# Kernel optimization log

Measured on AMD Instinct MI355X. Metric: run time of the kernel, lower is better.

## Reference

```python
import jax, jax.numpy as jnp
import numpy as np

NUM_NODES = 12
HEADS = 4
PERIOD = 24
HID = 144  # nn.LSTM(12*12, 12*12, 2)
NEG_INF = -9e15

ADJ = np.array([
    [1,0,0,0,0,1,0,0,0,0,1,1],
    [0,1,0,0,0,0,0,1,0,0,1,0],
    [0,0,1,0,0,0,1,0,0,0,0,1],
    [0,0,0,1,0,0,1,0,0,0,0,0],
    [0,0,0,0,1,1,0,0,0,0,0,0],
    [1,0,0,0,1,1,0,0,0,0,0,0],
    [0,0,1,1,0,0,1,0,0,0,1,0],
    [0,1,0,0,0,0,0,1,0,1,0,0],
    [0,0,0,0,0,0,0,0,1,1,1,1],
    [0,0,0,0,0,0,0,1,1,1,1,0],
    [1,1,0,0,0,0,1,0,1,1,1,1],
    [1,0,1,0,0,0,0,0,1,0,1,1]], dtype=np.int32)
EI, EJ = np.nonzero(ADJ)  # static edge list (row-major order, matches torch nonzero)


def gat_layer(x, W, b, a):
    # x: [B, N, c_in]; W: [c_in, H*c]; a: [H, 2c]
    B, N, _ = x.shape
    H = a.shape[0]
    h = (x @ W + b).reshape(B, N, H, -1)  # [B,N,H,c]
    # NOTE: adj has batch dim 1 in the original, so logits come from sample 0 only
    hi = h[0, EI]  # [E,H,c]
    hj = h[0, EJ]
    logits = jnp.einsum('ehc,hc->eh', jnp.concatenate([hi, hj], axis=-1), a)
    logits = jax.nn.leaky_relu(logits, 0.2)
    mat = jnp.full((N, N, H), NEG_INF, dtype=logits.dtype).at[EI, EJ].set(logits)
    probs = jax.nn.softmax(mat, axis=1)  # softmax over j (dim=2 in torch incl. batch)
    out = jnp.einsum('ijh,bjhc->bihc', probs, h)  # broadcast attn over batch
    return out.reshape(B, N, -1)  # concat heads


def lstm2(x, params, h0, c0):
    # x: [T,B,D]; params: list of (Wih,Whh,bih,bhh); h0,c0: [L,B,HID]
    hs, cs = [], []
    y = x
    for l, (Wih, Whh, bih, bhh) in enumerate(params):
        def step(carry, xt, Wih=Wih, Whh=Whh, bih=bih, bhh=bhh):
            h, c = carry
            g = xt @ Wih.T + h @ Whh.T + (bih + bhh)
            i, f, gg, o = jnp.split(g, 4, axis=-1)  # torch gate order i,f,g,o
            c2 = jax.nn.sigmoid(f) * c + jax.nn.sigmoid(i) * jnp.tanh(gg)
            h2 = jax.nn.sigmoid(o) * jnp.tanh(c2)
            return (h2, c2), h2
        (hT, cT), y = jax.lax.scan(step, (h0[l], c0[l]), y)
        hs.append(hT)
        cs.append(cT)
    return y, jnp.stack(hs), jnp.stack(cs)


def reference(x, gW0, gb0, ga0, gW1, gb1, ga1,
              eWih0, eWhh0, ebih0, ebhh0, eWih1, eWhh1, ebih1, ebhh1,
              dWih0, dWhh0, dbih0, dbhh0, dWih1, dWhh1, dbih1, dbhh1,
              gW3, gb3, ga3, gW4, gb4, ga4, fW, fb):
    B = x.shape[0]
    h = jax.nn.elu(gat_layer(x, gW0, gb0, ga0))           # [B,12,16]
    h = jax.nn.elu(gat_layer(h, gW1, gb1, ga1))           # [B,12,12]
    seq = h.reshape(PERIOD, -1, NUM_NODES * 12)            # [24, B/24, 144]
    Bb = seq.shape[1]
    z = jnp.zeros((2, Bb, HID), dtype=seq.dtype)
    enc_params = [(eWih0, eWhh0, ebih0, ebhh0), (eWih1, eWhh1, ebih1, ebhh1)]
    dec_params = [(dWih0, dWhh0, dbih0, dbhh0), (dWih1, dWhh1, dbih1, dbhh1)]
    y, hn, _ = lstm2(seq, enc_params, z, z)
    dec_in = jnp.zeros_like(y)
    y, _, _ = lstm2(dec_in, dec_params, hn, jnp.zeros_like(hn))
    h = y.reshape(-1, NUM_NODES, 12)                       # [B,12,12]
    h = jax.nn.elu(gat_layer(h, gW3, gb3, ga3))            # [B,12,16]
    h = jax.nn.elu(gat_layer(h, gW4, gb4, ga4))            # [B,12,24]
    h = h.reshape(B, NUM_NODES * 24)
    h = jax.nn.leaky_relu(h @ fW + fb, 0.01)               # fc_layers
    xr = h.reshape(B, NUM_NODES, -1)                       # [B,12,22]
    # F.mse_loss(..., reduce='sum') -> legacy truthy reduce => mean reduction
    out = jnp.mean((x - xr) ** 2, axis=(1, 2)).reshape(-1, 1)
    return out


def setup_inputs() -> dict:
    key = jax.random.key(0)
    ks = iter(jax.random.split(key, 64))
    def p(shape, s=0.2):
        return s * jax.random.normal(next(ks), shape, dtype=jnp.float32)
    B = 98304  # multiple of period=24
    d = {
        'x': jax.random.normal(next(ks), (B, 12, 22), dtype=jnp.float32),
        'gW0': p((22, 16)), 'gb0': p((16,)), 'ga0': p((4, 8)),
        'gW1': p((16, 12)), 'gb1': p((12,)), 'ga1': p((4, 6)),
    }
    for pre in ('e', 'd'):
        for l in (0, 1):
            d[f'{pre}Wih{l}'] = p((576, 144))
            d[f'{pre}Whh{l}'] = p((576, 144))
            d[f'{pre}bih{l}'] = p((576,))
            d[f'{pre}bhh{l}'] = p((576,))
    d.update({'gW3': p((12, 16)), 'gb3': p((16,)), 'ga3': p((4, 8)),
              'gW4': p((16, 24)), 'gb4': p((24,)), 'ga4': p((4, 12)),
              'fW': p((288, 264)), 'fb': p((264,))})
    return d
```

## Files before the change

kernel.cpp:

```cpp
#include <hip/hip_runtime.h>

#define DI __device__ __forceinline__

typedef short bfrag8 __attribute__((ext_vector_type(8)));
typedef float ffrag4 __attribute__((ext_vector_type(4)));

DI ushort f2b(float f){
  union { float f; unsigned u; } v; v.f = f;
  unsigned u = v.u;
  u += 0x7FFF + ((u >> 16) & 1);
  return (ushort)(u >> 16);
}
DI float b2f(ushort h){
  union { unsigned u; float f; } v; v.u = ((unsigned)h) << 16;
  return v.f;
}
DI float sigm(float x){ return 1.0f / (1.0f + __expf(-x)); }
DI float tanh_(float x){ return 1.0f - 2.0f / (1.0f + __expf(2.0f * x)); }
DI float elu_(float x){ return x > 0.f ? x : __expf(x) - 1.f; }

__global__ void k_probs(const float* xf, const ushort* xb, int in_c,
                        const float* W1, const float* b1, const float* a1, int hc1, int c1,
                        const float* W2, const float* b2, const float* a2, int hc2, int c2,
                        float* outA, float* outB)
{
  __shared__ float xs[12 * 22];
  __shared__ float h1[12 * 16];
  __shared__ float lg[4 * 144];
  __shared__ float pr[4 * 144];
  __shared__ float h1e[12 * 16];
  __shared__ float h2[12 * 24];
  const int t = threadIdx.x;
  const unsigned adj[12] = {0xC21u,0x482u,0x844u,0x048u,0x030u,0x031u,
                            0x44Cu,0x282u,0xF00u,0x780u,0xF43u,0xD05u};
  if (t < 12 * in_c){
    if (xf) xs[t] = xf[t];
    else    xs[t] = b2f(xb[t]);
  }
  __syncthreads();
  if (t < 12 * hc1){
    int i = t / hc1, o = t % hc1;
    float v = b1[o];
    for (int k = 0; k < in_c; k++) v += xs[i * in_c + k] * W1[k * hc1 + o];
    h1[t] = v;
  }
  __syncthreads();
  {
    int h = t / 144, ij = t % 144, i = ij / 12, j = ij % 12;
    float v;
    if ((adj[i] >> j) & 1){
      v = 0.f;
      for (int c = 0; c < c1; c++)
        v += a1[h*2*c1 + c] * h1[i*hc1 + h*c1 + c] + a1[h*2*c1 + c1 + c] * h1[j*hc1 + h*c1 + c];
      v = v > 0.f ? v : 0.2f * v;
    } else v = -9e15f;
    lg[t] = v;
  }
  __syncthreads();
  if (t < 48){
    int h = t / 12, i = t % 12;
    const float* row = &lg[h*144 + i*12];
    float m = row[0];
    for (int j = 1; j < 12; j++) m = fmaxf(m, row[j]);
    float e[12], s = 0.f;
    for (int j = 0; j < 12; j++){ e[j] = __expf(row[j] - m); s += e[j]; }
    float inv = 1.f / s;
    for (int j = 0; j < 12; j++){
      float p = e[j] * inv;
      pr[h*144 + i*12 + j] = p;
      outA[h*144 + i*12 + j] = p;
    }
  }
  __syncthreads();
  if (t < 12 * hc1){
    int i = t / hc1, o = t % hc1, h = o / c1;
    float v = 0.f;
    for (int j = 0; j < 12; j++) v += pr[h*144 + i*12 + j] * h1[j*hc1 + o];
    h1e[t] = elu_(v);
  }
  __syncthreads();
  if (t < 12 * hc2){
    int i = t / hc2, o = t % hc2;
    float v = b2[o];
    for (int k = 0; k < hc1; k++) v += h1e[i*hc1 + k] * W2[k*hc2 + o];
    h2[t] = v;
  }
  __syncthreads();
  {
    int h = t / 144, ij = t % 144, i = ij / 12, j = ij % 12;
    float v;
    if ((adj[i] >> j) & 1){
      v = 0.f;
      for (int c = 0; c < c2; c++)
        v += a2[h*2*c2 + c] * h2[i*hc2 + h*c2 + c] + a2[h*2*c2 + c2 + c] * h2[j*hc2 + h*c2 + c];
      v = v > 0.f ? v : 0.2f * v;
    } else v = -9e15f;
    lg[t] = v;
  }
  __syncthreads();
  if (t < 48){
    int h = t / 12, i = t % 12;
    const float* row = &lg[h*144 + i*12];
    float m = row[0];
    for (int j = 1; j < 12; j++) m = fmaxf(m, row[j]);
    float e[12], s = 0.f;
    for (int j = 0; j < 12; j++){ e[j] = __expf(row[j] - m); s += e[j]; }
    float inv = 1.f / s;
    for (int j = 0; j < 12; j++) outB[h*144 + i*12 + j] = e[j] * inv;
  }
}

__global__ void k_prep_op(const float* __restrict__ W, const float* __restrict__ p,
                          int Cin, int Cout, int hdiv, int K, int KT, int N,
                          ushort* __restrict__ dst)
{
  int bI = blockIdx.x;
  int kt = bI % KT, nt = bI / KT;
  int l = threadIdx.x, ln = l & 15, q = l >> 4;
  int n = nt * 16 + ln;
  for (int j = 0; j < 8; j++){
    int k = kt * 32 + q * 8 + j;
    float v = 0.f;
    if (k < K && n < N){
      if (p){
        int jj = k / Cin, kk = k % Cin;
        int i = n / Cout, o = n % Cout;
        v = p[(o / hdiv) * 144 + i * 12 + jj] * W[kk * Cout + o];
      } else {
        v = W[k * Cout + n];
      }
    }
    dst[((long)bI * 64 + l) * 8 + j] = f2b(v);
  }
}

__global__ void k_prep_lstm(const float* eWih0, const float* eWhh0,
                            const float* eWih1, const float* eWhh1,
                            const float* dWhh0,
                            const float* dWih1, const float* dWhh1,
                            ushort* __restrict__ dstBase)
{
  int combo = blockIdx.y;
  const float* Wh; const float* Wx; long off; int ntau;
  if (combo == 0){ Wh = eWhh0; Wx = eWih0; off = 0;      ntau = 72; }
  else if (combo == 1){ Wh = eWhh1; Wx = eWih1; off = 184320; ntau = 72; }
  else if (combo == 2){ Wh = dWhh0; Wx = dWhh0; off = 368640; ntau = 36; }
  else { Wh = dWhh1; Wx = dWih1; off = 460800; ntau = 72; }
  int bI = blockIdx.x;
  int tau = bI / 5, kt = bI % 5;
  if (tau >= ntau) return;
  const float* W = (tau < 36) ? Wh : Wx;
  int tt = (tau < 36) ? tau : tau - 36;
  int gt = tt / 9, ct = tt % 9;
  int l = threadIdx.x, ln = l & 15, q = l >> 4;
  int n = gt * 144 + ct * 16 + ln;
  ushort* d = dstBase + off;
  for (int j = 0; j < 8; j++){
    int k = kt * 32 + q * 8 + j;
    float v = (k < 144) ? W[(long)n * 144 + k] : 0.f;
    d[((long)bI * 64 + l) * 8 + j] = f2b(v);
  }
}

__global__ __launch_bounds__(512) void k_gat01(
    const float* __restrict__ x, const ushort* __restrict__ M0f, const float* __restrict__ b0,
    const ushort* __restrict__ M1f, const float* __restrict__ b1,
    ushort* __restrict__ seq)
{
  __shared__ ushort xs[128 * 288];
  __shared__ ushort h1e[128 * 200];
  int t = threadIdx.x;
  long row0 = (long)blockIdx.x * 128;
  int w = t >> 6, l = t & 63, q = l >> 4, ln = l & 15;
  if (t < 384){
    int row = t / 3, seg = t % 3;
    *(uint4*)&xs[row * 288 + 264 + seg * 8] = make_uint4(0u, 0u, 0u, 0u);
  }
  for (int idx = t; idx < 8448; idx += 512){
    int row = idx / 66, c4 = idx % 66;
    float4 v = *(const float4*)&x[(row0 + row) * 264 + c4 * 4];
    ushort4 o; o.x = f2b(v.x); o.y = f2b(v.y); o.z = f2b(v.z); o.w = f2b(v.w);
    *(ushort4*)&xs[row * 288 + c4 * 4] = o;
  }
  int nta[2] = {w, (w < 4) ? 8 + w : -1};
  bfrag8 f0[2][9];
  #pragma unroll
  for (int ii = 0; ii < 2; ii++)
    if (nta[ii] >= 0)
      #pragma unroll
      for (int kt = 0; kt < 9; kt++)
        f0[ii][kt] = *(const bfrag8*)&M0f[((long)(nta[ii] * 9 + kt) * 64 + l) * 8];
  float bias0 = b0[ln];
  __syncthreads();
  for (int rb = 0; rb < 8; rb++){
    bfrag8 af[9];
    #pragma unroll
    for (int kt = 0; kt < 9; kt++)
      af[kt] = *(const bfrag8*)&xs[(rb * 16 + ln) * 288 + kt * 32 + q * 8];
    #pragma unroll
    for (int ii = 0; ii < 2; ii++){
      if (nta[ii] < 0) continue;
      ffrag4 acc = {bias0, bias0, bias0, bias0};
      #pragma unroll
      for (int kt = 0; kt < 9; kt++)
        acc = __builtin_amdgcn_mfma_f32_16x16x32_bf16(af[kt], f0[ii][kt], acc, 0, 0, 0);
      #pragma unroll
      for (int r = 0; r < 4; r++)
        h1e[(rb * 16 + q * 4 + r) * 200 + nta[ii] * 16 + ln] = f2b(elu_(acc[r]));
    }
  }
  int ntb[2] = {w, (w == 0) ? 8 : -1};
  bfrag8 f1[2][6];
  #pragma unroll
  for (int ii = 0; ii < 2; ii++)
    if (ntb[ii] >= 0)
      #pragma unroll
      for (int kt = 0; kt < 6; kt++)
        f1[ii][kt] = *(const bfrag8*)&M1f[((long)(ntb[ii] * 6 + kt) * 64 + l) * 8];
  __syncthreads();
  for (int rb = 0; rb < 8; rb++){
    bfrag8 af[6];
    #pragma unroll
    for (int kt = 0; kt < 6; kt++)
      af[kt] = *(const bfrag8*)&h1e[(rb * 16 + ln) * 200 + kt * 32 + q * 8];
    #pragma unroll
    for (int ii = 0; ii < 2; ii++){
      if (ntb[ii] < 0) continue;
      int n = ntb[ii] * 16 + ln;
      float bias = b1[n % 12];
      ffrag4 acc = {bias, bias, bias, bias};
      #pragma unroll
      for (int kt = 0; kt < 6; kt++)
        acc = __builtin_amdgcn_mfma_f32_16x16x32_bf16(af[kt], f1[ii][kt], acc, 0, 0, 0);
      #pragma unroll
      for (int r = 0; r < 4; r++)
        xs[(rb * 16 + q * 4 + r) * 144 + n] = f2b(elu_(acc[r]));
    }
  }
  __syncthreads();
  for (int i = t; i < 2304; i += 512)
    *(uint4*)&seq[row0 * 144 + (long)i * 8] = *(uint4*)&xs[i * 8];
}

template<bool HASX>
__global__ __launch_bounds__(512, 2) void k_scan(
    const ushort* __restrict__ Wf,
    const ushort* __restrict__ seqin,
    const float* __restrict__ bih, const float* __restrict__ bhh,
    const ushort* __restrict__ h0,
    ushort* __restrict__ Y,
    ushort* __restrict__ hT)
{
  constexpr int NT = HASX ? 9 : 5;
  __shared__ ushort hl[16 * 168];
  __shared__ float P[(HASX ? 2 : 1) * 9216];
  __shared__ float bsh[576];
  int t = threadIdx.x, rbk = blockIdx.x;
  int w = t >> 6, l = t & 63, q = l >> 4, ln = l & 15;
  if (t < 336){
    int row = t / 21, ch = t % 21;
    uint4 z = make_uint4(0u, 0u, 0u, 0u);
    if (h0 && ch < 18) z = *(const uint4*)&h0[((long)rbk * 16 + row) * 144 + ch * 8];
    *(uint4*)&hl[row * 168 + ch * 8] = z;
  }
  for (int i = t; i < 576; i += 512) bsh[i] = bih[i] + bhh[i];
  bfrag8 wf[NT][5];
  #pragma unroll
  for (int i = 0; i < NT; i++){
    int tau = w + i * 8;
    int tc = (HASX || tau < 36) ? tau : 0;
    #pragma unroll
    for (int kt = 0; kt < 5; kt++)
      wf[i][kt] = *(const bfrag8*)&Wf[((long)(tc * 5 + kt) * 64 + l) * 8];
  }
  float cst[5] = {0.f, 0.f, 0.f, 0.f, 0.f};
  __syncthreads();
  for (int ts = 0; ts < 24; ts++){
    bfrag8 ah[5];
    #pragma unroll
    for (int kt = 0; kt < 5; kt++)
      ah[kt] = *(const bfrag8*)&hl[ln * 168 + kt * 32 + q * 8];
    bfrag8 ax[5];
    if (HASX){
      const ushort* xr = &seqin[(((long)ts * 4096) + (long)rbk * 16 + ln) * 144];
      #pragma unroll
      for (int kt = 0; kt < 5; kt++)
        ax[kt] = *(const bfrag8*)&xr[kt * 32 + q * 8];
    }
    #pragma unroll
    for (int i = 0; i < NT; i++){
      int tau = w + i * 8;
      if (!HASX && tau >= 36) continue;
      ffrag4 acc = {0.f, 0.f, 0.f, 0.f};
      if (HASX && tau >= 36){
        #pragma unroll
        for (int kt = 0; kt < 5; kt++)
          acc = __builtin_amdgcn_mfma_f32_16x16x32_bf16(ax[kt], wf[i][kt], acc, 0, 0, 0);
        int tt = tau - 36;
        *(float4*)&P[9216 + ((tt / 9) * 144 + (tt % 9) * 16 + ln) * 16 + q * 4] = *(float4*)&acc;
      } else {
        #pragma unroll
        for (int kt = 0; kt < 5; kt++)
          acc = __builtin_amdgcn_mfma_f32_16x16x32_bf16(ah[kt], wf[i][kt], acc, 0, 0, 0);
        *(float4*)&P[((tau / 9) * 144 + (tau % 9) * 16 + ln) * 16 + q * 4] = *(float4*)&acc;
      }
    }
    __syncthreads();
    #pragma unroll
    for (int j = 0; j < 5; j++){
      int cell = t + j * 512;
      if (cell < 2304){
        int col = cell >> 4, row = cell & 15;
        int base = col * 16 + row;
        float iv = P[base], fv = P[2304 + base], gv = P[4608 + base], ov = P[6912 + base];
        if (HASX){
          iv += P[9216 + base]; fv += P[9216 + 2304 + base];
          gv += P[9216 + 4608 + base]; ov += P[9216 + 6912 + base];
        }
        iv += bsh[col]; fv += bsh[144 + col]; gv += bsh[288 + col]; ov += bsh[432 + col];
        float cn = sigm(fv) * cst[j] + sigm(iv) * tanh_(gv);
        cst[j] = cn;
        hl[row * 168 + col] = f2b(sigm(ov) * tanh_(cn));
      }
    }
    __syncthreads();
    if (Y && t < 288){
      int row = t / 18, ch = t % 18;
      *(uint4*)&Y[(((long)ts * 4096) + (long)rbk * 16 + row) * 144 + ch * 8] =
          *(uint4*)&hl[row * 168 + ch * 8];
    }
  }
  if (hT && t < 288){
    int row = t / 18, ch = t % 18;
    *(uint4*)&hT[((long)rbk * 16 + row) * 144 + ch * 8] = *(uint4*)&hl[row * 168 + ch * 8];
  }
}

__global__ __launch_bounds__(512) void k_tail(
    const ushort* __restrict__ Ya, const ushort* __restrict__ M3f, const float* __restrict__ b3,
    const ushort* __restrict__ M4f, const float* __restrict__ b4,
    const ushort* __restrict__ fWt, const float* __restrict__ fb,
    const float* __restrict__ x, float* __restrict__ out)
{
  __shared__ ushort h3e[128 * 200];
  __shared__ ushort bufB[128 * 288];
  __shared__ float psum[128 * 8];
  ushort* ys = bufB;
  ushort* h4e = bufB;
  int t = threadIdx.x;
  long row0 = (long)blockIdx.x * 128;
  int w = t >> 6, l = t & 63, q = l >> 4, ln = l & 15;
  if (t < 256){
    int row = t / 2, seg = t % 2;
    *(uint4*)&ys[row * 160 + 144 + seg * 8] = make_uint4(0u, 0u, 0u, 0u);
  }
  for (int idx = t; idx < 2304; idx += 512){
    int row = idx / 18, ch = idx % 18;
    *(uint4*)&ys[row * 160 + ch * 8] = *(const uint4*)&Ya[(row0 + row) * 144 + (long)ch * 8];
  }
  int nta[2] = {w, (w < 4) ? 8 + w : -1};
  bfrag8 f3[2][5];
  #pragma unroll
  for (int ii = 0; ii < 2; ii++)
    if (nta[ii] >= 0)
      #pragma unroll
      for (int kt = 0; kt < 5; kt++)
        f3[ii][kt] = *(const bfrag8*)&M3f[((long)(nta[ii] * 5 + kt) * 64 + l) * 8];
  float bias3 = b3[ln];
  __syncthreads();
  for (int rb = 0; rb < 8; rb++){
    bfrag8 af[5];
    #pragma unroll
    for (int kt = 0; kt < 5; kt++)
      af[kt] = *(const bfrag8*)&ys[(rb * 16 + ln) * 160 + kt * 32 + q * 8];
    #pragma unroll
    for (int ii = 0; ii < 2; ii++){
      if (nta[ii] < 0) continue;
      ffrag4 acc = {bias3, bias3, bias3, bias3};
      #pragma unroll
      for (int kt = 0; kt < 5; kt++)
        acc = __builtin_amdgcn_mfma_f32_16x16x32_bf16(af[kt], f3[ii][kt], acc, 0, 0, 0);
      #pragma unroll
      for (int r = 0; r < 4; r++)
        h3e[(rb * 16 + q * 4 + r) * 200 + nta[ii] * 16 + ln] = f2b(elu_(acc[r]));
    }
  }
  int ntb[3] = {2 * w, 2 * w + 1, (w < 2) ? 16 + w : -1};
  bfrag8 f4[3][6];
  #pragma unroll
  for (int ii = 0; ii < 3; ii++)
    if (ntb[ii] >= 0)
      #pragma unroll
      for (int kt = 0; kt < 6; kt++)
        f4[ii][kt] = *(const bfrag8*)&M4f[((long)(ntb[ii] * 6 + kt) * 64 + l) * 8];
  __syncthreads();
  for (int rb = 0; rb < 8; rb++){
    bfrag8 af[6];
    #pragma unroll
    for (int kt = 0; kt < 6; kt++)
      af[kt] = *(const bfrag8*)&h3e[(rb * 16 + ln) * 200 + kt * 32 + q * 8];
    #pragma unroll
    for (int ii = 0; ii < 3; ii++){
      if (ntb[ii] < 0) continue;
      int n = ntb[ii] * 16 + ln;
      float bias = b4[n % 24];
      ffrag4 acc = {bias, bias, bias, bias};
      #pragma unroll
      for (int kt = 0; kt < 6; kt++)
        acc = __builtin_amdgcn_mfma_f32_16x16x32_bf16(af[kt], f4[ii][kt], acc, 0, 0, 0);
      #pragma unroll
      for (int r = 0; r < 4; r++)
        h4e[(rb * 16 + q * 4 + r) * 288 + n] = f2b(elu_(acc[r]));
    }
  }
  int ntc[3] = {2 * w, 2 * w + 1, (w == 0) ? 16 : -1};
  bfrag8 f5[3][9];
  float bias5[3] = {0.f, 0.f, 0.f};
  #pragma unroll
  for (int ii = 0; ii < 3; ii++)
    if (ntc[ii] >= 0){
      #pragma unroll
      for (int kt = 0; kt < 9; kt++)
        f5[ii][kt] = *(const bfrag8*)&fWt[((long)(ntc[ii] * 9 + kt) * 64 + l) * 8];
      int n = ntc[ii] * 16 + ln;
      bias5[ii] = (n < 264) ? fb[n] : 0.f;
    }
  __syncthreads();
  for (int rb = 0; rb < 8; rb++){
    bfrag8 af[9];
    #pragma unroll
    for (int kt = 0; kt < 9; kt++)
      af[kt] = *(const bfrag8*)&h4e[(rb * 16 + ln) * 288 + kt * 32 + q * 8];
    float s4[4] = {0.f, 0.f, 0.f, 0.f};
    #pragma unroll
    for (int ii = 0; ii < 3; ii++){
      if (ntc[ii] < 0) continue;
      ffrag4 acc = {bias5[ii], bias5[ii], bias5[ii], bias5[ii]};
      #pragma unroll
      for (int kt = 0; kt < 9; kt++)
        acc = __builtin_amdgcn_mfma_f32_16x16x32_bf16(af[kt], f5[ii][kt], acc, 0, 0, 0);
      int n = ntc[ii] * 16 + ln;
      if (n < 264){
        #pragma unroll
        for (int r = 0; r < 4; r++){
          float v = acc[r];
          v = v > 0.f ? v : 0.01f * v;
          long row = row0 + rb * 16 + q * 4 + r;
          float d = x[row * 264 + n] - v;
          s4[r] += d * d;
        }
      }
    }
    #pragma unroll
    for (int off = 1; off < 16; off <<= 1){
      #pragma unroll
      for (int r = 0; r < 4; r++) s4[r] += __shfl_xor(s4[r], off, 16);
    }
    if (ln == 0){
      #pragma unroll
      for (int r = 0; r < 4; r++) psum[(rb * 16 + q * 4 + r) * 8 + w] = s4[r];
    }
  }
  __syncthreads();
  if (t < 128){
    float s = 0.f;
    for (int k = 0; k < 8; k++) s += psum[t * 8 + k];
    out[row0 + t] = s * (1.0f / 264.0f);
  }
}

extern "C" void kernel_launch(void* const* d_in, const int* in_sizes, int n_in,
                              void* d_out, int out_size, void* d_ws, size_t ws_size,
                              hipStream_t stream)
{
  const float* x     = (const float*)d_in[0];
  const float* gW0   = (const float*)d_in[1];
  const float* gb0   = (const float*)d_in[2];
  const float* ga0   = (const float*)d_in[3];
  const float* gW1   = (const float*)d_in[4];
  const float* gb1   = (const float*)d_in[5];
  const float* ga1   = (const float*)d_in[6];
  const float* eWih0 = (const float*)d_in[7];
  const float* eWhh0 = (const float*)d_in[8];
  const float* ebih0 = (const float*)d_in[9];
  const float* ebhh0 = (const float*)d_in[10];
  const float* eWih1 = (const float*)d_in[11];
  const float* eWhh1 = (const float*)d_in[12];
  const float* ebih1 = (const float*)d_in[13];
  const float* ebhh1 = (const float*)d_in[14];
  const float* dWhh0 = (const float*)d_in[16];
  const float* dbih0 = (const float*)d_in[17];
  const float* dbhh0 = (const float*)d_in[18];
  const float* dWih1 = (const float*)d_in[19];
  const float* dWhh1 = (const float*)d_in[20];
  const float* dbih1 = (const float*)d_in[21];
  const float* dbhh1 = (const float*)d_in[22];
  const float* gW3   = (const float*)d_in[23];
  const float* gb3   = (const float*)d_in[24];
  const float* ga3   = (const float*)d_in[25];
  const float* gW4   = (const float*)d_in[26];
  const float* gb4   = (const float*)d_in[27];
  const float* ga4   = (const float*)d_in[28];
  const float* fW    = (const float*)d_in[29];
  const float* fb    = (const float*)d_in[30];

  char* ws = (char*)d_ws;
  float*  probs0 = (float*)(ws + 0);
  float*  probs1 = (float*)(ws + 2304);
  float*  probs3 = (float*)(ws + 4608);
  float*  probs4 = (float*)(ws + 6912);
  ushort* M0f    = (ushort*)(ws + 9216);
  ushort* M1f    = (ushort*)(ws + 119808);
  ushort* M3f    = (ushort*)(ws + 175104);
  ushort* M4f    = (ushort*)(ws + 236544);
  ushort* fWt    = (ushort*)(ws + 347136);
  ushort* lstmF  = (ushort*)(ws + 503808);
  ushort* seq    = (ushort*)(ws + 1794048);
  ushort* Ya     = (ushort*)(ws + 30105600);
  ushort* Yb     = (ushort*)(ws + 58417152);
  ushort* hT0    = (ushort*)(ws + 86728704);
  ushort* hT1    = (ushort*)(ws + 87908352);
  float* out = (float*)d_out;

  k_prep_lstm<<<dim3(360, 4), 64, 0, stream>>>(eWih0, eWhh0, eWih1, eWhh1,
                                               dWhh0, dWih1, dWhh1, lstmF);
  k_prep_op<<<153, 64, 0, stream>>>(fW, nullptr, 0, 264, 1, 288, 9, 264, fWt);
  k_probs<<<1, 576, 0, stream>>>(x, nullptr, 22,
                                 gW0, gb0, ga0, 16, 4,
                                 gW1, gb1, ga1, 12, 3,
                                 probs0, probs1);
  k_prep_op<<<108, 64, 0, stream>>>(gW0, probs0, 22, 16, 4, 264, 9, 192, M0f);
  k_prep_op<<<54, 64, 0, stream>>>(gW1, probs1, 16, 12, 3, 192, 6, 144, M1f);
  k_gat01<<<768, 512, 0, stream>>>(x, M0f, gb0, M1f, gb1, seq);

  k_scan<true><<<256, 512, 0, stream>>>(lstmF + 0L,      seq, ebih0, ebhh0, nullptr, Ya, hT0);
  k_scan<true><<<256, 512, 0, stream>>>(lstmF + 184320L, Ya, ebih1, ebhh1, nullptr, nullptr, hT1);
  k_scan<false><<<256, 512, 0, stream>>>(lstmF + 368640L, nullptr, dbih0, dbhh0, hT0, Yb, nullptr);
  k_scan<true><<<256, 512, 0, stream>>>(lstmF + 460800L, Yb, dbih1, dbhh1, hT1, Ya, nullptr);

  k_probs<<<1, 576, 0, stream>>>(nullptr, Ya, 12,
                                 gW3, gb3, ga3, 16, 4,
                                 gW4, gb4, ga4, 24, 6,
                                 probs3, probs4);
  k_prep_op<<<60, 64, 0, stream>>>(gW3, probs3, 12, 16, 4, 144, 5, 192, M3f);
  k_prep_op<<<108, 64, 0, stream>>>(gW4, probs4, 16, 24, 6, 192, 6, 288, M4f);
  k_tail<<<768, 512, 0, stream>>>(Ya, M3f, gb3, M4f, gb4, fWt, fb, x, out);
}
```

Before: 669.1 us.

## Warp-specialize LSTM scan: overlap input projection with recurrent gate math

The LSTM scan kernel is split into two warp groups. Four warps hold the recurrent weights and compute the gates and cell update in registers straight from the MFMA accumulators. The other four warps precompute the input projection plus bias for the next timestep into a double-buffered shared array, prefetching sequence rows two steps ahead. This removes the full shared-memory gate round trip and the second elementwise pass, and moves the x-projection off the recurrent critical path. In exchange it uses more registers per thread and more shared memory, and Y is now written as scattered 2-byte global stores instead of vectorized rows.

```diff
diff --git a/kernel.cpp b/kernel.cpp
--- a/kernel.cpp
+++ b/kernel.cpp
@@ -251,88 +251,149 @@
     ushort* __restrict__ Y,
     ushort* __restrict__ hT)
 {
-  constexpr int NT = HASX ? 9 : 5;
-  __shared__ ushort hl[16 * 168];
-  __shared__ float P[(HASX ? 2 : 1) * 9216];
-  __shared__ float bsh[576];
+  __shared__ float Px[2][11520];
+  __shared__ float P8[1280];
+  __shared__ ushort hl[2][2688];
   int t = threadIdx.x, rbk = blockIdx.x;
   int w = t >> 6, l = t & 63, q = l >> 4, ln = l & 15;
   if (t < 336){
     int row = t / 21, ch = t % 21;
     uint4 z = make_uint4(0u, 0u, 0u, 0u);
     if (h0 && ch < 18) z = *(const uint4*)&h0[((long)rbk * 16 + row) * 144 + ch * 8];
-    *(uint4*)&hl[row * 168 + ch * 8] = z;
-  }
-  for (int i = t; i < 576; i += 512) bsh[i] = bih[i] + bhh[i];
-  bfrag8 wf[NT][5];
-  #pragma unroll
-  for (int i = 0; i < NT; i++){
-    int tau = w + i * 8;
-    int tc = (HASX || tau < 36) ? tau : 0;
+    *(uint4*)&hl[0][row * 168 + ch * 8] = z;
+    *(uint4*)&hl[1][row * 168 + ch * 8] = make_uint4(0u, 0u, 0u, 0u);
+  }
+  if (w < 4){
+    bfrag8 wh[2][4][5], w8[5];
+    #pragma unroll
+    for (int ci = 0; ci < 2; ci++)
+      #pragma unroll
+      for (int gt = 0; gt < 4; gt++)
+        #pragma unroll
+        for (int kt = 0; kt < 5; kt++)
+          wh[ci][gt][kt] = *(const bfrag8*)&Wf[((long)((gt * 9 + 2 * w + ci) * 5 + kt) * 64 + l) * 8];
     #pragma unroll
     for (int kt = 0; kt < 5; kt++)
-      wf[i][kt] = *(const bfrag8*)&Wf[((long)(tc * 5 + kt) * 64 + l) * 8];
-  }
-  float cst[5] = {0.f, 0.f, 0.f, 0.f, 0.f};
-  __syncthreads();
-  for (int ts = 0; ts < 24; ts++){
-    bfrag8 ah[5];
-    #pragma unroll
-    for (int kt = 0; kt < 5; kt++)
-      ah[kt] = *(const bfrag8*)&hl[ln * 168 + kt * 32 + q * 8];
-    bfrag8 ax[5];
+      w8[kt] = *(const bfrag8*)&Wf[((long)((w * 9 + 8) * 5 + kt) * 64 + l) * 8];
+    float cst[2][4] = {};
+    float c8 = 0.f;
+    __syncthreads();
+    for (int ts = 0; ts < 24; ts++){
+      int par = ts & 1;
+      const ushort* hlr = &hl[par][0];
+      ushort* hlw = &hl[par ^ 1][0];
+      bfrag8 ah[5];
+      #pragma unroll
+      for (int kt = 0; kt < 5; kt++)
+        ah[kt] = *(const bfrag8*)&hlr[ln * 168 + kt * 32 + q * 8];
+      #pragma unroll
+      for (int ci = 0; ci < 2; ci++){
+        int ct = 2 * w + ci;
+        ffrag4 acc[4];
+        #pragma unroll
+        for (int gt = 0; gt < 4; gt++)
+          acc[gt] = *(ffrag4*)&Px[par][(gt * 144 + ct * 16 + ln) * 20 + q * 4];
+        #pragma unroll
+        for (int gt = 0; gt < 4; gt++)
+          #pragma unroll
+          for (int kt = 0; kt < 5; kt++)
+            acc[gt] = __builtin_amdgcn_mfma_f32_16x16x32_bf16(ah[kt], wh[ci][gt][kt], acc[gt], 0, 0, 0);
+        #pragma unroll
+        for (int r = 0; r < 4; r++){
+          float cn = sigm(acc[1][r]) * cst[ci][r] + sigm(acc[0][r]) * tanh_(acc[2][r]);
+          cst[ci][r] = cn;
+          ushort hb = f2b(sigm(acc[3][r]) * tanh_(cn));
+          hlw[(q * 4 + r) * 168 + ct * 16 + ln] = hb;
+          if (Y) Y[(((long)ts * 4096) + rbk * 16 + q * 4 + r) * 144 + ct * 16 + ln] = hb;
+        }
+      }
+      {
+        ffrag4 a8 = *(ffrag4*)&Px[par][(w * 144 + 128 + ln) * 20 + q * 4];
+        #pragma unroll
+        for (int kt = 0; kt < 5; kt++)
+          a8 = __builtin_amdgcn_mfma_f32_16x16x32_bf16(ah[kt], w8[kt], a8, 0, 0, 0);
+        *(ffrag4*)&P8[(w * 16 + ln) * 20 + q * 4] = a8;
+      }
+      __syncthreads();
+      if (t < 256){
+        int row = t >> 4, c8c = t & 15;
+        float iv = P8[(0 * 16 + c8c) * 20 + row];
+        float fv = P8[(1 * 16 + c8c) * 20 + row];
+        float gv = P8[(2 * 16 + c8c) * 20 + row];
+        float ov = P8[(3 * 16 + c8c) * 20 + row];
+        float cn = sigm(fv) * c8 + sigm(iv) * tanh_(gv);
+        c8 = cn;
+        ushort hb = f2b(sigm(ov) * tanh_(cn));
+        hl[par ^ 1][row * 168 + 128 + c8c] = hb;
+        if (Y) Y[(((long)ts * 4096) + rbk * 16 + row) * 144 + 128 + c8c] = hb;
+      }
+      __syncthreads();
+    }
+  } else {
+    int j = w - 4;
+    bfrag8 wx[9][5];
+    float biasx[9];
+    #pragma unroll
+    for (int i = 0; i < 9; i++){
+      int n = j * 144 + i * 16 + ln;
+      biasx[i] = bih[n] + bhh[n];
+      if (HASX)
+        #pragma unroll
+        for (int kt = 0; kt < 5; kt++)
+          wx[i][kt] = *(const bfrag8*)&Wf[((long)((36 + j * 9 + i) * 5 + kt) * 64 + l) * 8];
+    }
+    bfrag8 axc[5];
     if (HASX){
-      const ushort* xr = &seqin[(((long)ts * 4096) + (long)rbk * 16 + ln) * 144];
+      const ushort* xr = &seqin[((long)rbk * 16 + ln) * 144];
       #pragma unroll
       for (int kt = 0; kt < 5; kt++)
-        ax[kt] = *(const bfrag8*)&xr[kt * 32 + q * 8];
-    }
-    #pragma unroll
-    for (int i = 0; i < NT; i++){
-      int tau = w + i * 8;
-      if (!HASX && tau >= 36) continue;
-      ffrag4 acc = {0.f, 0.f, 0.f, 0.f};
-      if (HASX && tau >= 36){
+        axc[kt] = *(const bfrag8*)&xr[kt * 32 + q * 8];
+      #pragma unroll
+      for (int i = 0; i < 9; i++){
+        ffrag4 acc = {biasx[i], biasx[i], biasx[i], biasx[i]};
         #pragma unroll
         for (int kt = 0; kt < 5; kt++)
-          acc = __builtin_amdgcn_mfma_f32_16x16x32_bf16(ax[kt], wf[i][kt], acc, 0, 0, 0);
-        int tt = tau - 36;
-        *(float4*)&P[9216 + ((tt / 9) * 144 + (tt % 9) * 16 + ln) * 16 + q * 4] = *(float4*)&acc;
-      } else {
-        #pragma unroll
-        for (int kt = 0; kt < 5; kt++)
-          acc = __builtin_amdgcn_mfma_f32_16x16x32_bf16(ah[kt], wf[i][kt], acc, 0, 0, 0);
-        *(float4*)&P[((tau / 9) * 144 + (tau % 9) * 16 + ln) * 16 + q * 4] = *(float4*)&acc;
+          acc = __builtin_amdgcn_mfma_f32_16x16x32_bf16(axc[kt], wx[i][kt], acc, 0, 0, 0);
+        *(ffrag4*)&Px[0][(j * 144 + i * 16 + ln) * 20 + q * 4] = acc;
+      }
+      const ushort* xr1 = &seqin[(4096L + (long)rbk * 16 + ln) * 144];
+      #pragma unroll
+      for (int kt = 0; kt < 5; kt++)
+        axc[kt] = *(const bfrag8*)&xr1[kt * 32 + q * 8];
+    } else {
+      #pragma unroll
+      for (int i = 0; i < 9; i++){
+        ffrag4 acc = {biasx[i], biasx[i], biasx[i], biasx[i]};
+        *(ffrag4*)&Px[0][(j * 144 + i * 16 + ln) * 20 + q * 4] = acc;
+        *(ffrag4*)&Px[1][(j * 144 + i * 16 + ln) * 20 + q * 4] = acc;
       }
     }
     __syncthreads();
-    #pragma unroll
-    for (int j = 0; j < 5; j++){
-      int cell = t + j * 512;
-      if (cell < 2304){
-        int col = cell >> 4, row = cell & 15;
-        int base = col * 16 + row;
-        float iv = P[base], fv = P[2304 + base], gv = P[4608 + base], ov = P[6912 + base];
-        if (HASX){
-          iv += P[9216 + base]; fv += P[9216 + 2304 + base];
-          gv += P[9216 + 4608 + base]; ov += P[9216 + 6912 + base];
+    for (int ts = 0; ts < 24; ts++){
+      if (HASX && ts < 23){
+        int par = ts & 1;
+        #pragma unroll
+        for (int i = 0; i < 9; i++){
+          ffrag4 acc = {biasx[i], biasx[i], biasx[i], biasx[i]};
+          #pragma unroll
+          for (int kt = 0; kt < 5; kt++)
+            acc = __builtin_amdgcn_mfma_f32_16x16x32_bf16(axc[kt], wx[i][kt], acc, 0, 0, 0);
+          *(ffrag4*)&Px[par ^ 1][(j * 144 + i * 16 + ln) * 20 + q * 4] = acc;
         }
-        iv += bsh[col]; fv += bsh[144 + col]; gv += bsh[288 + col]; ov += bsh[432 + col];
-        float cn = sigm(fv) * cst[j] + sigm(iv) * tanh_(gv);
-        cst[j] = cn;
-        hl[row * 168 + col] = f2b(sigm(ov) * tanh_(cn));
-      }
-    }
-    __syncthreads();
-    if (Y && t < 288){
-      int row = t / 18, ch = t % 18;
-      *(uint4*)&Y[(((long)ts * 4096) + (long)rbk * 16 + row) * 144 + ch * 8] =
-          *(uint4*)&hl[row * 168 + ch * 8];
+        if (ts < 22){
+          const ushort* xr = &seqin[(((long)(ts + 2)) * 4096 + (long)rbk * 16 + ln) * 144];
+          #pragma unroll
+          for (int kt = 0; kt < 5; kt++)
+            axc[kt] = *(const bfrag8*)&xr[kt * 32 + q * 8];
+        }
+      }
+      __syncthreads();
+      __syncthreads();
     }
   }
   if (hT && t < 288){
     int row = t / 18, ch = t % 18;
-    *(uint4*)&hT[((long)rbk * 16 + row) * 144 + ch * 8] = *(uint4*)&hl[row * 168 + ch * 8];
+    *(uint4*)&hT[((long)rbk * 16 + row) * 144 + ch * 8] = *(uint4*)&hl[0][row * 168 + ch * 8];
   }
 }
 
```

Result: faster. 598.2 us (-10.6%).
